# Performance work log

Hardware: AMD Instinct MI355X
Metric: run time of the kernel (lower is better)

Reference implementation:

```python
import jax, jax.numpy as jnp
import numpy as np

D_MODEL, N_HEADS, RANK = 1024, 16, 32
HEAD_DIM = D_MODEL // N_HEADS
B, S = 4, 2048


def setup_inputs() -> dict:
    key = jax.random.key(0)
    ks = jax.random.split(key, 8)
    inp = {
        "x": jax.random.normal(ks[0], (B, S, D_MODEL), dtype=jnp.float32),
        "mask": jnp.ones((B, S), dtype=jnp.int32),
        "qkv_u": jax.random.normal(ks[1], (D_MODEL, RANK), jnp.float32) / D_MODEL ** 0.5,
        "qkv_v": jax.random.normal(ks[2], (RANK, 3 * D_MODEL), jnp.float32) / RANK ** 0.5,
        "qkv_b": jnp.zeros((3 * D_MODEL,), jnp.float32),
        "u_attn": jax.random.normal(ks[3], (N_HEADS, HEAD_DIM, RANK), jnp.float32) / HEAD_DIM ** 0.5,
        "v_attn": jax.random.normal(ks[4], (N_HEADS, RANK, HEAD_DIM), jnp.float32) / RANK ** 0.5,
        "out_u": jax.random.normal(ks[5], (D_MODEL, RANK), jnp.float32) / D_MODEL ** 0.5,
        "out_v": jax.random.normal(ks[6], (RANK, D_MODEL), jnp.float32) / RANK ** 0.5,
        "out_b": jnp.zeros((D_MODEL,), jnp.float32),
    }
    return inp


def reference(x, mask, qkv_u, qkv_v, qkv_b, u_attn, v_attn, out_u, out_v, out_b):
    bs, seq_len, d_model = x.shape
    n_heads, head_dim, rank = u_attn.shape
    scale = 1.0 / jnp.sqrt(jnp.float32(rank))

    # Low-rank QKV projection: [B,S,3D]
    qkv = (x @ qkv_u) @ qkv_v + qkv_b
    q, k, v = jnp.split(qkv, 3, axis=-1)

    def to_heads(t):  # [B,S,D] -> [B,H,S,hd]
        return t.reshape(bs, seq_len, n_heads, head_dim).transpose(0, 2, 1, 3)

    q, k, v = to_heads(q), to_heads(k), to_heads(v)

    # Rank-projected Q/K: [B,H,S,r]
    q_low = jnp.einsum("bhsd,hdr->bhsr", q, u_attn)
    k_low = jnp.einsum("bhtd,hdr->bhtr", k, u_attn)
    scores = jnp.einsum("bhsr,bhtr->bhst", q_low, k_low) * scale

    # mask: [B,S] keys; masked_fill where mask == 0
    scores = jnp.where(mask[:, None, None, :] == 0, jnp.float32(-jnp.inf), scores)
    attn = jax.nn.softmax(scores, axis=-1)  # dropout is identity in eval

    v_low = jnp.einsum("bhtd,hdr->bhtr", v, u_attn)
    context_low = jnp.einsum("bhst,bhtr->bhsr", attn, v_low)
    context = jnp.einsum("bhsr,hrd->bhsd", context_low, v_attn)
    context = context.transpose(0, 2, 1, 3).reshape(bs, seq_len, d_model)

    return (context @ out_u) @ out_v + out_b
```

## Files before the change

### kernel.cpp

```cpp
#include <hip/hip_runtime.h>
#include <hip/hip_bf16.h>

typedef unsigned int u32;
typedef unsigned short u16;
typedef __attribute__((ext_vector_type(8))) __bf16 bf16x8;
typedef __attribute__((ext_vector_type(16))) float f32x16;
typedef __attribute__((ext_vector_type(2))) unsigned int u32x2;

#define QSCALE 0.25505418f
#define MFMA __builtin_amdgcn_mfma_f32_32x32x16_bf16


static __device__ __forceinline__ u16 f2b(float f) {
  __hip_bfloat16 h = __float2bfloat16(f);
  return *reinterpret_cast<u16*>(&h);
}
static __device__ __forceinline__ u32 cvtpk(float lo, float hi) {
  u32 r;
  asm("v_cvt_pk_bf16_f32 %0, %1, %2" : "=v"(r) : "v"(lo), "v"(hi));
  return r;
}

static __device__ __forceinline__ float xhalf_sum(float v) {
#if __has_builtin(__builtin_amdgcn_permlane32_swap)
  u32 a = __float_as_uint(v);
  u32x2 r = __builtin_amdgcn_permlane32_swap(a, a, false, false);
  return __uint_as_float(r[0]) + __uint_as_float(r[1]);
#else
  return v + __shfl_xor(v, 32);
#endif
}

static __device__ __forceinline__ int tau(int p) {
  int g = p >> 2;
  int gk = (g & 4) | ((g & 1) << 1) | ((g >> 1) & 1);
  return (gk << 2) | (p & 3);
}

static __device__ __forceinline__ int fmoff(int row, int col) {
  return (col >> 4) * 512 + (((col >> 3) & 1) * 32 + (row & 31)) * 8 + (col & 7);
}

__global__ __launch_bounds__(256) void k_prep(const float* __restrict__ qkv_v,
                                              const float* __restrict__ qkv_b,
                                              const float* __restrict__ u_attn,
                                              const float* __restrict__ v_attn,
                                              const float* __restrict__ out_u,
                                              const float* __restrict__ qkv_u,
                                              const float* __restrict__ out_v,
                                              u16* __restrict__ WQF, u16* __restrict__ WKF,
                                              u16* __restrict__ WVF, float* __restrict__ BQKV,
                                              u16* __restrict__ WOTF, u16* __restrict__ UTF,
                                              u16* __restrict__ OVF) {
  int blk = blockIdx.x;
  int tid = threadIdx.x;
  if (blk < 16) {
    int h = blk;
    int r = tid & 31, g = tid >> 5;
    for (int rp = g; rp < 32; rp += 8) {
      float aq = 0.f, ak = 0.f, av = 0.f;
      for (int d = 0; d < 64; ++d) {
        float u = u_attn[(h * 64 + d) * 32 + r];
        aq += qkv_v[rp * 3072 + h * 64 + d] * u;
        ak += qkv_v[rp * 3072 + 1024 + h * 64 + d] * u;
        av += qkv_v[rp * 3072 + 2048 + h * 64 + d] * u;
      }
      int o = h * 1024 + fmoff(r, rp);
      WQF[o] = f2b(aq);
      WKF[o] = f2b(ak);
      WVF[o] = f2b(av);
    }
    for (int rr = g; rr < 32; rr += 8) {
      float a = 0.f;
      for (int d = 0; d < 64; ++d)
        a += v_attn[(h * 32 + rr) * 64 + d] * out_u[(h * 64 + d) * 32 + r];
      WOTF[fmoff(r, h * 32 + rr)] = f2b(a);
    }
    if (tid < 32) {
      float aq = 0.f, ak = 0.f, av = 0.f;
      for (int d = 0; d < 64; ++d) {
        float u = u_attn[(h * 64 + d) * 32 + r];
        aq += qkv_b[h * 64 + d] * u;
        ak += qkv_b[1024 + h * 64 + d] * u;
        av += qkv_b[2048 + h * 64 + d] * u;
      }
      BQKV[h * 32 + r] = aq;
      BQKV[512 + h * 32 + r] = ak;
      BQKV[1024 + h * 32 + r] = av;
    }
  } else if (blk < 24) {
    int kb = (blk - 16) * 128;
    for (int i = tid; i < 4096; i += 256) {
      int r = i >> 7, kl = i & 127;
      int k = kb + kl;
      UTF[fmoff(r, k)] = f2b(qkv_u[k * 32 + r]);
    }
  } else {
    int db = (blk - 24) * 128;
    for (int i = tid; i < 4096; i += 256) {
      int dl = i >> 5, r = i & 31;
      int d = db + dl;
      OVF[(d >> 5) * 1024 + fmoff(d, r)] = f2b(out_v[r * 1024 + d]);
    }
  }
}

__global__ __launch_bounds__(512) void k_proj(const float* __restrict__ x,
                                              const u16* __restrict__ UTF,
                                              u16* __restrict__ TF) {
  __shared__ float xl[32][129];
  __shared__ float red[8][32][33];
  int tid = threadIdx.x;
  int w = tid >> 6, l = tid & 63, lo = l & 31, hi = l >> 5;
  int m0 = blockIdx.x * 32;
  int srow = tid >> 4, scol = (tid & 15) * 8;
  const float* xp = x + (size_t)(m0 + srow) * 1024 + scol;
  f32x16 acc = {};
  for (int ch = 0; ch < 8; ++ch) {
    float4 x0 = *(const float4*)(xp);
    float4 x1 = *(const float4*)(xp + 4);
    xp += 128;
    xl[srow][scol + 0] = x0.x;
    xl[srow][scol + 1] = x0.y;
    xl[srow][scol + 2] = x0.z;
    xl[srow][scol + 3] = x0.w;
    xl[srow][scol + 4] = x1.x;
    xl[srow][scol + 5] = x1.y;
    xl[srow][scol + 6] = x1.z;
    xl[srow][scol + 7] = x1.w;
    __syncthreads();
    const float* src = &xl[lo][w * 16 + hi * 8];
    union { bf16x8 v; u32 u[4]; } af;
    af.u[0] = cvtpk(src[0], src[1]);
    af.u[1] = cvtpk(src[2], src[3]);
    af.u[2] = cvtpk(src[4], src[5]);
    af.u[3] = cvtpk(src[6], src[7]);
    bf16x8 bf = *(const bf16x8*)(UTF + (ch * 8 + w) * 512 + l * 8);
    acc = MFMA(af.v, bf, acc, 0, 0, 0);
    __syncthreads();
  }
#pragma unroll
  for (int i = 0; i < 16; ++i)
    red[w][(i & 3) + 8 * (i >> 2) + 4 * hi][lo] = acc[i];
  __syncthreads();
  int m = tid >> 4, c = (tid & 15) * 2;
  float v0 = 0.f, v1 = 0.f;
#pragma unroll
  for (int ww = 0; ww < 8; ++ww) {
    v0 += red[ww][m][c + 0];
    v1 += red[ww][m][c + 1];
  }
  *(u32*)(TF + (size_t)blockIdx.x * 1024 + fmoff(m, c)) = cvtpk(v0, v1);
}

__global__ __launch_bounds__(256) void k_lowproj(const u16* __restrict__ TF,
                                                 const u16* __restrict__ WQF,
                                                 const u16* __restrict__ WKF,
                                                 const u16* __restrict__ WVF,
                                                 const float* __restrict__ BQKV,
                                                 u16* __restrict__ QLF, u16* __restrict__ KF,
                                                 u16* __restrict__ VF) {
  __shared__ float vtf[32][132];
  int tid = threadIdx.x;
  int w = tid >> 6, l = tid & 63, lo = l & 31, hi = l >> 5;
  int blk = blockIdx.x;
  int bh = blk >> 4, sb = (blk & 15) * 128;
  int b = bh >> 4, h = bh & 15;
  int qt = (sb >> 5) + w;

  const u16* wq = WQF + h * 1024 + l * 8;
  const u16* wk = WKF + h * 1024 + l * 8;
  const u16* wv = WVF + h * 1024 + l * 8;
  bf16x8 aq0 = *(const bf16x8*)(wq), aq1 = *(const bf16x8*)(wq + 512);
  bf16x8 ak0 = *(const bf16x8*)(wk), ak1 = *(const bf16x8*)(wk + 512);
  bf16x8 av0 = *(const bf16x8*)(wv), av1 = *(const bf16x8*)(wv + 512);

  const u16* tp = TF + (size_t)(b * 64 + qt) * 1024 + l * 8;
  bf16x8 tb0 = *(const bf16x8*)(tp), tb1 = *(const bf16x8*)(tp + 512);

  f32x16 cq = {}, ck = {}, cv = {};
  cq = MFMA(aq0, tb0, cq, 0, 0, 0);
  cq = MFMA(aq1, tb1, cq, 0, 0, 0);
  ck = MFMA(ak0, tb0, ck, 0, 0, 0);
  ck = MFMA(ak1, tb1, ck, 0, 0, 0);
  cv = MFMA(av0, tb0, cv, 0, 0, 0);
  cv = MFMA(av1, tb1, cv, 0, 0, 0);

  size_t qbase = (size_t)bh * 65536 + (size_t)qt * 1024;
  size_t tbase = (size_t)bh * 65536 + (size_t)qt * 1024;
  int slp = w * 32 + tau(lo);
#pragma unroll
  for (int g2 = 0; g2 < 4; ++g2) {
    float4 bq4 = *(const float4*)(BQKV + h * 32 + g2 * 8 + 4 * hi);
    float4 bk4 = *(const float4*)(BQKV + 512 + h * 32 + g2 * 8 + 4 * hi);
    float4 bv4 = *(const float4*)(BQKV + 1024 + h * 32 + g2 * 8 + 4 * hi);
    float q0 = (cq[4 * g2 + 0] + bq4.x) * QSCALE;
    float q1 = (cq[4 * g2 + 1] + bq4.y) * QSCALE;
    float q2 = (cq[4 * g2 + 2] + bq4.z) * QSCALE;
    float q3 = (cq[4 * g2 + 3] + bq4.w) * QSCALE;
    uint2 qo; qo.x = cvtpk(q0, q1); qo.y = cvtpk(q2, q3);
    *(uint2*)(QLF + qbase + (g2 >> 1) * 512 + ((g2 & 1) * 32 + lo) * 8 + 4 * hi) = qo;
    uint2 ko;
    ko.x = cvtpk(ck[4 * g2 + 0] + bk4.x, ck[4 * g2 + 1] + bk4.y);
    ko.y = cvtpk(ck[4 * g2 + 2] + bk4.z, ck[4 * g2 + 3] + bk4.w);
    *(uint2*)(KF + tbase + (g2 >> 1) * 512 + (g2 & 1) * 256 + lo * 8 + 4 * hi) = ko;
    int rbase = g2 * 8 + 4 * hi;
    vtf[rbase + 0][slp] = cv[4 * g2 + 0] + bv4.x;
    vtf[rbase + 1][slp] = cv[4 * g2 + 1] + bv4.y;
    vtf[rbase + 2][slp] = cv[4 * g2 + 2] + bv4.z;
    vtf[rbase + 3][slp] = cv[4 * g2 + 3] + bv4.w;
  }
  __syncthreads();
  for (int u = tid; u < 512; u += 256) {
    int r = u >> 4, su = (u & 15) * 8;
    const float* src = &vtf[r][su];
    uint4 o;
    o.x = cvtpk(src[0], src[1]);
    o.y = cvtpk(src[2], src[3]);
    o.z = cvtpk(src[4], src[5]);
    o.w = cvtpk(src[6], src[7]);
    int c = su & 31, tloc = su >> 5;
    *(uint4*)(VF + (size_t)bh * 65536 + (size_t)((sb >> 5) + tloc) * 1024 +
              (c >> 4) * 512 + ((c >> 3) & 1) * 256 + r * 8) = o;
  }
}

__global__ __launch_bounds__(256) void k_attn(const u16* __restrict__ QLF,
                                              const u16* __restrict__ KF,
                                              const u16* __restrict__ VF,
                                              const int* __restrict__ mask,
                                              u16* __restrict__ CTX2) {
  __shared__ float pacc[2][64][17];
  __shared__ float pl[2][64];
  __shared__ u32 cls[64][17];
  int tid = threadIdx.x;
  int wave = tid >> 6, l = tid & 63, lo = l & 31, hi = l >> 5;
  int blk = blockIdx.x;
  int xcd = blk & 7, slot = blk >> 3;
  int bh = xcd * 8 + (slot >> 5);
  int qpair = slot & 31;
  int qi = wave & 1;
  int khalf = wave >> 1;
  int qt = qpair * 2 + qi;
  int b = bh >> 4, h = bh & 15;

  const int* mk = mask + b * 2048;

  const u16* qp = QLF + (size_t)bh * 65536 + (size_t)qt * 1024 + l * 8;
  bf16x8 qb0 = *(const bf16x8*)(qp);
  bf16x8 qb1 = *(const bf16x8*)(qp + 512);

  size_t fbase = (size_t)bh * 65536 + (size_t)khalf * 32768 + l * 8;
  const u16* kp = KF + fbase;
  const u16* vp = VF + fbase;

  f32x16 acc = {};
  float l_run = 0.f;

  int mall = 1;
  for (int i = l; i < 2048; i += 64) mall &= (mk[i] != 0) ? 1 : 0;

  if (__all(mall)) {
#pragma unroll 1
    for (int kt = 0; kt < 32; ++kt) {
      bf16x8 ka0 = *(const bf16x8*)(kp);
      bf16x8 ka1 = *(const bf16x8*)(kp + 512);
      kp += 1024;
      f32x16 sc = {};
      sc = MFMA(ka0, qb0, sc, 0, 0, 0);
      sc = MFMA(ka1, qb1, sc, 0, 0, 0);
      bf16x8 va0 = *(const bf16x8*)(vp);
      bf16x8 va1 = *(const bf16x8*)(vp + 512);
      vp += 1024;
      union { bf16x8 v; u32 u[4]; } fa;
      float a0 = __builtin_amdgcn_exp2f(sc[0]);
      float a1 = __builtin_amdgcn_exp2f(sc[1]);
      float a2 = __builtin_amdgcn_exp2f(sc[2]);
      float a3 = __builtin_amdgcn_exp2f(sc[3]);
      fa.u[0] = cvtpk(a0, a1);
      fa.u[1] = cvtpk(a2, a3);
      float t0 = (a0 + a1) + (a2 + a3);
      a0 = __builtin_amdgcn_exp2f(sc[4]);
      a1 = __builtin_amdgcn_exp2f(sc[5]);
      a2 = __builtin_amdgcn_exp2f(sc[6]);
      a3 = __builtin_amdgcn_exp2f(sc[7]);
      fa.u[2] = cvtpk(a0, a1);
      fa.u[3] = cvtpk(a2, a3);
      float t1 = (a0 + a1) + (a2 + a3);
      acc = MFMA(va0, fa.v, acc, 0, 0, 0);
      union { bf16x8 v; u32 u[4]; } fc;
      a0 = __builtin_amdgcn_exp2f(sc[8]);
      a1 = __builtin_amdgcn_exp2f(sc[9]);
      a2 = __builtin_amdgcn_exp2f(sc[10]);
      a3 = __builtin_amdgcn_exp2f(sc[11]);
      fc.u[0] = cvtpk(a0, a1);
      fc.u[1] = cvtpk(a2, a3);
      float t2 = (a0 + a1) + (a2 + a3);
      a0 = __builtin_amdgcn_exp2f(sc[12]);
      a1 = __builtin_amdgcn_exp2f(sc[13]);
      a2 = __builtin_amdgcn_exp2f(sc[14]);
      a3 = __builtin_amdgcn_exp2f(sc[15]);
      fc.u[2] = cvtpk(a0, a1);
      fc.u[3] = cvtpk(a2, a3);
      float t3 = (a0 + a1) + (a2 + a3);
      acc = MFMA(va1, fc.v, acc, 0, 0, 0);
      l_run += (t0 + t1) + (t2 + t3);
    }
  } else {
    const int* mp = mk + khalf * 1024 + lo;
#pragma unroll 1
    for (int kt = 0; kt < 32; ++kt) {
      unsigned long long bm = __ballot(mp[0] != 0);
      mp += 32;
      bf16x8 ka0 = *(const bf16x8*)(kp);
      bf16x8 ka1 = *(const bf16x8*)(kp + 512);
      kp += 1024;
      f32x16 sc = {};
      sc = MFMA(ka0, qb0, sc, 0, 0, 0);
      sc = MFMA(ka1, qb1, sc, 0, 0, 0);
      u32 km = (u32)bm;
#pragma unroll
      for (int i = 0; i < 16; ++i) {
        int key = (i & 3) + 8 * (i >> 2) + 4 * hi;
        if (!((km >> key) & 1)) sc[i] = -3.0e38f;
      }
      bf16x8 va0 = *(const bf16x8*)(vp);
      bf16x8 va1 = *(const bf16x8*)(vp + 512);
      vp += 1024;
      union { bf16x8 v; u32 u[4]; } fa;
      float a0 = __builtin_amdgcn_exp2f(sc[0]);
      float a1 = __builtin_amdgcn_exp2f(sc[1]);
      float a2 = __builtin_amdgcn_exp2f(sc[2]);
      float a3 = __builtin_amdgcn_exp2f(sc[3]);
      fa.u[0] = cvtpk(a0, a1);
      fa.u[1] = cvtpk(a2, a3);
      float t0 = (a0 + a1) + (a2 + a3);
      a0 = __builtin_amdgcn_exp2f(sc[4]);
      a1 = __builtin_amdgcn_exp2f(sc[5]);
      a2 = __builtin_amdgcn_exp2f(sc[6]);
      a3 = __builtin_amdgcn_exp2f(sc[7]);
      fa.u[2] = cvtpk(a0, a1);
      fa.u[3] = cvtpk(a2, a3);
      float t1 = (a0 + a1) + (a2 + a3);
      acc = MFMA(va0, fa.v, acc, 0, 0, 0);
      union { bf16x8 v; u32 u[4]; } fc;
      a0 = __builtin_amdgcn_exp2f(sc[8]);
      a1 = __builtin_amdgcn_exp2f(sc[9]);
      a2 = __builtin_amdgcn_exp2f(sc[10]);
      a3 = __builtin_amdgcn_exp2f(sc[11]);
      fc.u[0] = cvtpk(a0, a1);
      fc.u[1] = cvtpk(a2, a3);
      float t2 = (a0 + a1) + (a2 + a3);
      a0 = __builtin_amdgcn_exp2f(sc[12]);
      a1 = __builtin_amdgcn_exp2f(sc[13]);
      a2 = __builtin_amdgcn_exp2f(sc[14]);
      a3 = __builtin_amdgcn_exp2f(sc[15]);
      fc.u[2] = cvtpk(a0, a1);
      fc.u[3] = cvtpk(a2, a3);
      float t3 = (a0 + a1) + (a2 + a3);
      acc = MFMA(va1, fc.v, acc, 0, 0, 0);
      l_run += (t0 + t1) + (t2 + t3);
    }
  }

  if (khalf) {
#pragma unroll
    for (int i = 0; i < 16; ++i) pacc[qi][l][i] = acc[i];
    pl[qi][l] = l_run;
  }
  __syncthreads();
  if (!khalf) {
#pragma unroll
    for (int i = 0; i < 16; ++i) acc[i] += pacc[qi][l][i];
    l_run += pl[qi][l];
    l_run = xhalf_sum(l_run);
    float inv = 1.0f / l_run;
    int qloc = qi * 32 + lo;
#pragma unroll
    for (int g2 = 0; g2 < 4; ++g2) {
      cls[qloc][g2 * 4 + 2 * hi] = cvtpk(acc[4 * g2 + 0] * inv, acc[4 * g2 + 1] * inv);
      cls[qloc][g2 * 4 + 2 * hi + 1] = cvtpk(acc[4 * g2 + 2] * inv, acc[4 * g2 + 3] * inv);
    }
  }
  __syncthreads();
  int st2 = tid >> 7, kcl = (tid >> 6) & 1, lw = tid & 63;
  const u32* src = &cls[st2 * 32 + (lw & 31)][kcl * 8 + (lw >> 5) * 4];
  uint4 v0;
  v0.x = src[0]; v0.y = src[1]; v0.z = src[2]; v0.w = src[3];
  *(uint4*)(CTX2 + (size_t)(b * 64 + qpair * 2 + st2) * 16384 +
            (2 * h + kcl) * 512 + lw * 8) = v0;
}

__global__ __launch_bounds__(512) void k_epi1(const u16* __restrict__ CTX2,
                                              const u16* __restrict__ WOTF,
                                              u16* __restrict__ YLF) {
  __shared__ float red[8][32][33];
  int tid = threadIdx.x;
  int w = tid >> 6, l = tid & 63, lo = l & 31, hi = l >> 5;
  int stile = blockIdx.x;
  const u16* cp = CTX2 + (size_t)stile * 16384 + (4 * w) * 512 + l * 8;
  const u16* wp = WOTF + (4 * w) * 512 + l * 8;
  f32x16 acc = {};
  for (int st = 0; st < 4; ++st) {
    bf16x8 a = *(const bf16x8*)(cp);
    bf16x8 bb = *(const bf16x8*)(wp);
    cp += 512;
    wp += 512;
    acc = MFMA(a, bb, acc, 0, 0, 0);
  }
#pragma unroll
  for (int i = 0; i < 16; ++i)
    red[w][(i & 3) + 8 * (i >> 2) + 4 * hi][lo] = acc[i];
  __syncthreads();
  int m = tid >> 4, c = (tid & 15) * 2;
  float v0 = 0.f, v1 = 0.f;
#pragma unroll
  for (int ww = 0; ww < 8; ++ww) {
    v0 += red[ww][m][c + 0];
    v1 += red[ww][m][c + 1];
  }
  *(u32*)(YLF + (size_t)stile * 1024 + fmoff(m, c)) = cvtpk(v0, v1);
}

__global__ __launch_bounds__(256) void k_epi2(const u16* __restrict__ YLF,
                                              const u16* __restrict__ OVF,
                                              const float* __restrict__ out_b,
                                              float* __restrict__ out) {
  __shared__ float ol[32][133];
  int tid = threadIdx.x;
  int w = tid >> 6, l = tid & 63, lo = l & 31, hi = l >> 5;
  int blk = blockIdx.x;
  int stile = blk >> 3;
  int s0 = stile * 32;
  int d0 = (blk & 7) * 128;
  int dtile = (blk & 7) * 4 + w;
  const u16* ap = OVF + (size_t)dtile * 1024 + l * 8;
  bf16x8 a0 = *(const bf16x8*)(ap), a1 = *(const bf16x8*)(ap + 512);
  const u16* bp = YLF + (size_t)stile * 1024 + l * 8;
  bf16x8 b0 = *(const bf16x8*)(bp), b1 = *(const bf16x8*)(bp + 512);
  f32x16 acc = {};
  acc = MFMA(a0, b0, acc, 0, 0, 0);
  acc = MFMA(a1, b1, acc, 0, 0, 0);
#pragma unroll
  for (int i = 0; i < 16; ++i)
    ol[lo][w * 32 + (i & 3) + 8 * (i >> 2) + 4 * hi] = acc[i];
  __syncthreads();
  for (int u = tid; u < 1024; u += 256) {
    int s = u >> 5, c = (u & 31) * 4;
    float4 ob = *(const float4*)(out_b + d0 + c);
    float4 o;
    o.x = ol[s][c + 0] + ob.x;
    o.y = ol[s][c + 1] + ob.y;
    o.z = ol[s][c + 2] + ob.z;
    o.w = ol[s][c + 3] + ob.w;
    *(float4*)(out + (size_t)(s0 + s) * 1024 + d0 + c) = o;
  }
}

extern "C" void kernel_launch(void* const* d_in, const int* in_sizes, int n_in,
                              void* d_out, int out_size, void* d_ws, size_t ws_size,
                              hipStream_t stream) {
  const float* x = (const float*)d_in[0];
  const int* mask = (const int*)d_in[1];
  const float* qkv_u = (const float*)d_in[2];
  const float* qkv_v = (const float*)d_in[3];
  const float* qkv_b = (const float*)d_in[4];
  const float* u_attn = (const float*)d_in[5];
  const float* v_attn = (const float*)d_in[6];
  const float* out_u = (const float*)d_in[7];
  const float* out_v = (const float*)d_in[8];
  const float* out_b = (const float*)d_in[9];
  float* out = (float*)d_out;

  char* w = (char*)d_ws;
  u16* WQF = (u16*)(w + 0);
  u16* WKF = (u16*)(w + (32 << 10));
  u16* WVF = (u16*)(w + (64 << 10));
  float* BQ = (float*)(w + (96 << 10));
  u16* WOTF = (u16*)(w + (104 << 10));
  u16* UTF = (u16*)(w + (136 << 10));
  u16* OVF = (u16*)(w + (200 << 10));
  u16* TF = (u16*)(w + (1 << 20));
  u16* QLF = (u16*)(w + (2 << 20));
  u16* KF = (u16*)(w + (10 << 20));
  u16* VF = (u16*)(w + (18 << 20));
  u16* CTX2 = (u16*)(w + (26 << 20));
  u16* YLF = (u16*)(w + (34 << 20));

  k_prep<<<32, 256, 0, stream>>>(qkv_v, qkv_b, u_attn, v_attn, out_u, qkv_u, out_v,
                                 WQF, WKF, WVF, BQ, WOTF, UTF, OVF);
  k_proj<<<256, 512, 0, stream>>>(x, UTF, TF);
  k_lowproj<<<1024, 256, 0, stream>>>(TF, WQF, WKF, WVF, BQ, QLF, KF, VF);
  k_attn<<<2048, 256, 0, stream>>>(QLF, KF, VF, mask, CTX2);
  k_epi1<<<256, 512, 0, stream>>>(CTX2, WOTF, YLF);
  k_epi2<<<2048, 256, 0, stream>>>(YLF, OVF, out_b, out);
}
```

Before: 115.1 us.

## Precompute global mask flag in prep kernel and double-buffer x tiles in projection

Adds a 33rd block to the prep kernel that scans the whole mask once and writes a single all-ones flag. The attention kernel now reads that flag instead of having every block rescan its 2048-entry mask row. The projection kernel also double-buffers its x shared-memory tile and prefetches the next chunk into registers, dropping one barrier per iteration. The global flag is stricter than the old per-batch check, so if any batch has a masked key, every batch takes the slower masked path.

Result: faster. 112.0 us (median of 2 runs) (-2.7%).

```diff
diff --git a/kernel.cpp b/kernel.cpp
--- a/kernel.cpp
+++ b/kernel.cpp
@@ -48,10 +48,12 @@
                                               const float* __restrict__ out_u,
                                               const float* __restrict__ qkv_u,
                                               const float* __restrict__ out_v,
+                                              const int* __restrict__ mask,
                                               u16* __restrict__ WQF, u16* __restrict__ WKF,
                                               u16* __restrict__ WVF, float* __restrict__ BQKV,
                                               u16* __restrict__ WOTF, u16* __restrict__ UTF,
-                                              u16* __restrict__ OVF) {
+                                              u16* __restrict__ OVF, int* __restrict__ flag) {
+  __shared__ int mred[4];
   int blk = blockIdx.x;
   int tid = threadIdx.x;
   if (blk < 16) {
@@ -95,41 +97,49 @@
       int k = kb + kl;
       UTF[fmoff(r, k)] = f2b(qkv_u[k * 32 + r]);
     }
-  } else {
+  } else if (blk < 32) {
     int db = (blk - 24) * 128;
     for (int i = tid; i < 4096; i += 256) {
       int dl = i >> 5, r = i & 31;
       int d = db + dl;
       OVF[(d >> 5) * 1024 + fmoff(d, r)] = f2b(out_v[r * 1024 + d]);
     }
+  } else {
+    int mall = 1;
+    for (int i = tid; i < 8192; i += 256) mall &= (mask[i] != 0) ? 1 : 0;
+    int wa = __all(mall) ? 1 : 0;
+    if ((tid & 63) == 0) mred[tid >> 6] = wa;
+    __syncthreads();
+    if (tid == 0) flag[0] = mred[0] & mred[1] & mred[2] & mred[3];
   }
 }
 
 __global__ __launch_bounds__(512) void k_proj(const float* __restrict__ x,
                                               const u16* __restrict__ UTF,
                                               u16* __restrict__ TF) {
-  __shared__ float xl[32][129];
+  __shared__ float xl[2][32][129];
   __shared__ float red[8][32][33];
   int tid = threadIdx.x;
   int w = tid >> 6, l = tid & 63, lo = l & 31, hi = l >> 5;
   int m0 = blockIdx.x * 32;
   int srow = tid >> 4, scol = (tid & 15) * 8;
   const float* xp = x + (size_t)(m0 + srow) * 1024 + scol;
+  float4 r0 = *(const float4*)(xp);
+  float4 r1 = *(const float4*)(xp + 4);
+  xp += 128;
   f32x16 acc = {};
   for (int ch = 0; ch < 8; ++ch) {
-    float4 x0 = *(const float4*)(xp);
-    float4 x1 = *(const float4*)(xp + 4);
-    xp += 128;
-    xl[srow][scol + 0] = x0.x;
-    xl[srow][scol + 1] = x0.y;
-    xl[srow][scol + 2] = x0.z;
-    xl[srow][scol + 3] = x0.w;
-    xl[srow][scol + 4] = x1.x;
-    xl[srow][scol + 5] = x1.y;
-    xl[srow][scol + 6] = x1.z;
-    xl[srow][scol + 7] = x1.w;
+    int buf = ch & 1;
+    float* dst = &xl[buf][srow][scol];
+    dst[0] = r0.x; dst[1] = r0.y; dst[2] = r0.z; dst[3] = r0.w;
+    dst[4] = r1.x; dst[5] = r1.y; dst[6] = r1.z; dst[7] = r1.w;
+    if (ch < 7) {
+      r0 = *(const float4*)(xp);
+      r1 = *(const float4*)(xp + 4);
+      xp += 128;
+    }
     __syncthreads();
-    const float* src = &xl[lo][w * 16 + hi * 8];
+    const float* src = &xl[buf][lo][w * 16 + hi * 8];
     union { bf16x8 v; u32 u[4]; } af;
     af.u[0] = cvtpk(src[0], src[1]);
     af.u[1] = cvtpk(src[2], src[3]);
@@ -137,7 +147,6 @@
     af.u[3] = cvtpk(src[6], src[7]);
     bf16x8 bf = *(const bf16x8*)(UTF + (ch * 8 + w) * 512 + l * 8);
     acc = MFMA(af.v, bf, acc, 0, 0, 0);
-    __syncthreads();
   }
 #pragma unroll
   for (int i = 0; i < 16; ++i)
@@ -229,6 +238,7 @@
                                               const u16* __restrict__ KF,
                                               const u16* __restrict__ VF,
                                               const int* __restrict__ mask,
+                                              const int* __restrict__ flag,
                                               u16* __restrict__ CTX2) {
   __shared__ float pacc[2][64][17];
   __shared__ float pl[2][64];
@@ -244,8 +254,6 @@
   int qt = qpair * 2 + qi;
   int b = bh >> 4, h = bh & 15;
 
-  const int* mk = mask + b * 2048;
-
   const u16* qp = QLF + (size_t)bh * 65536 + (size_t)qt * 1024 + l * 8;
   bf16x8 qb0 = *(const bf16x8*)(qp);
   bf16x8 qb1 = *(const bf16x8*)(qp + 512);
@@ -257,10 +265,7 @@
   f32x16 acc = {};
   float l_run = 0.f;
 
-  int mall = 1;
-  for (int i = l; i < 2048; i += 64) mall &= (mk[i] != 0) ? 1 : 0;
-
-  if (__all(mall)) {
+  if (flag[0]) {
 #pragma unroll 1
     for (int kt = 0; kt < 32; ++kt) {
       bf16x8 ka0 = *(const bf16x8*)(kp);
@@ -307,7 +312,7 @@
       l_run += (t0 + t1) + (t2 + t3);
     }
   } else {
-    const int* mp = mk + khalf * 1024 + lo;
+    const int* mp = mask + b * 2048 + khalf * 1024 + lo;
 #pragma unroll 1
     for (int kt = 0; kt < 32; ++kt) {
       unsigned long long bm = __ballot(mp[0] != 0);
@@ -477,6 +482,7 @@
   u16* WKF = (u16*)(w + (32 << 10));
   u16* WVF = (u16*)(w + (64 << 10));
   float* BQ = (float*)(w + (96 << 10));
+  int* FLAG = (int*)(w + (102 << 10));
   u16* WOTF = (u16*)(w + (104 << 10));
   u16* UTF = (u16*)(w + (136 << 10));
   u16* OVF = (u16*)(w + (200 << 10));
@@ -487,11 +493,11 @@
   u16* CTX2 = (u16*)(w + (26 << 20));
   u16* YLF = (u16*)(w + (34 << 20));
 
-  k_prep<<<32, 256, 0, stream>>>(qkv_v, qkv_b, u_attn, v_attn, out_u, qkv_u, out_v,
-                                 WQF, WKF, WVF, BQ, WOTF, UTF, OVF);
+  k_prep<<<33, 256, 0, stream>>>(qkv_v, qkv_b, u_attn, v_attn, out_u, qkv_u, out_v,
+                                 mask, WQF, WKF, WVF, BQ, WOTF, UTF, OVF, FLAG);
   k_proj<<<256, 512, 0, stream>>>(x, UTF, TF);
   k_lowproj<<<1024, 256, 0, stream>>>(TF, WQF, WKF, WVF, BQ, QLF, KF, VF);
-  k_attn<<<2048, 256, 0, stream>>>(QLF, KF, VF, mask, CTX2);
+  k_attn<<<2048, 256, 0, stream>>>(QLF, KF, VF, mask, FLAG, CTX2);
   k_epi1<<<256, 512, 0, stream>>>(CTX2, WOTF, YLF);
   k_epi2<<<2048, 256, 0, stream>>>(YLF, OVF, out_b, out);
 }
```
